# Kernel tuning notes

Hardware: AMD Instinct MI355X
Metric: run time of the kernel (lower is better)

The kernel has to match this reference:

```python
import jax, jax.numpy as jnp
import numpy as np

COMMITMENT_COST = 0.25


def setup_inputs() -> dict:
    key = jax.random.key(0)
    k1, k2 = jax.random.split(key)
    B, C, H, W, D = 8, 64, 32, 32, 32
    NUM_EMB = 512
    x = jax.random.normal(k1, (B, C, H, W, D), dtype=jnp.float32)
    # torch init: uniform(-1/num_embeddings, 1/num_embeddings)
    codebook = jax.random.uniform(k2, (NUM_EMB, C), dtype=jnp.float32,
                                  minval=-1.0 / NUM_EMB, maxval=1.0 / NUM_EMB)
    return {"x": x, "codebook": codebook}


def reference(x, codebook):
    B, C, H, W, D = x.shape
    # [B,C,H,W,D] -> [N, C] with N = B*H*W*D
    flat = jnp.transpose(x, (0, 2, 3, 4, 1)).reshape(-1, C)
    # squared L2 distances to every codebook entry: [N, num_embeddings]
    dist = (jnp.sum(flat * flat, axis=1, keepdims=True)
            - 2.0 * flat @ codebook.T
            + jnp.sum(codebook * codebook, axis=1))
    idx = jnp.argmin(dist, axis=1)                     # [N]
    # one-hot @ codebook  ==  gather (same math, efficient form)
    quant_flat = codebook[idx]                          # [N, C]
    quant = jnp.transpose(quant_flat.reshape(B, H, W, D, C), (0, 4, 1, 2, 3))
    e_loss = jnp.mean((jax.lax.stop_gradient(quant) - x) ** 2)
    q_loss = jnp.mean((quant - jax.lax.stop_gradient(x)) ** 2)
    loss = q_loss + COMMITMENT_COST * e_loss
    # straight-through estimator
    quant_st = x + jax.lax.stop_gradient(quant - x)
    return quant_st, loss
```

## Files before the change

### kernel.cpp

```cpp
#include <hip/hip_runtime.h>
#include <cstdint>
#include <cstddef>

#define SPATIAL   32768
#define CHANNELS  64
#define NUM_EMB   512
#define NPOS      262144
#define OUT_ELEMS 16777216
#define BLOCK     256
#define LOSS_SCALE (1.25f / 16777216.0f)

typedef __attribute__((ext_vector_type(8))) short bf16x8;
typedef __attribute__((ext_vector_type(4))) float f32x4;

union b8u { int i[4]; bf16x8 v; };
union fiu { float f; unsigned u; };

__device__ __forceinline__ short f2bf_rne(float f) {
    fiu v; v.f = f;
    unsigned r = v.u + 0x7fffu + ((v.u >> 16) & 1u);
    return (short)(r >> 16);
}

__global__ void vq_prep(const float* __restrict__ cb,
                        short* __restrict__ cbbf,
                        float* __restrict__ cbn,
                        float* __restrict__ loss_slot) {
    int e = blockIdx.x * blockDim.x + threadIdx.x;
    if (e == 0) *loss_slot = 0.0f;
    if (e < NUM_EMB) {
        float s = 0.0f;
#pragma unroll
        for (int c = 0; c < CHANNELS; ++c) {
            float v = cb[e * CHANNELS + c];
            cbbf[e * CHANNELS + c] = f2bf_rne(v);
            s = __builtin_fmaf(v, v, s);
        }
        cbn[e] = -0.5f * s;
    }
}

__global__ __launch_bounds__(BLOCK) void vq_main(
    const float* __restrict__ x,
    const float* __restrict__ cb,
    const short* __restrict__ cbbf,
    const float* __restrict__ cbn,
    float* __restrict__ out,
    float* __restrict__ loss_slot) {
#pragma clang fp contract(off)
    __shared__ int   cand[BLOCK];
    __shared__ float wsum[4];

    const int tid  = threadIdx.x;
    const int wave = tid >> 6, lane = tid & 63;
    const int q    = lane >> 4, col = lane & 15;

    const int blockPos = blockIdx.x * BLOCK;
    const int b     = blockPos >> 15;
    const int sbase = blockPos & 32767;
    const float* xb = x + (size_t)b * (CHANNELS * SPATIAL);
    const int wbase = sbase + wave * 64;

    b8u A[4][2];
#pragma unroll
    for (int t = 0; t < 4; ++t) {
        const unsigned* pu = (const unsigned*)xb + (wbase + t * 16 + col);
#pragma unroll
        for (int kh = 0; kh < 2; ++kh) {
#pragma unroll
            for (int jj = 0; jj < 4; ++jj) {
                unsigned u0 = pu[(size_t)(kh * 32 + q * 8 + 2 * jj + 0) * SPATIAL];
                unsigned u1 = pu[(size_t)(kh * 32 + q * 8 + 2 * jj + 1) * SPATIAL];
                A[t][kh].i[jj] = __builtin_amdgcn_perm(u1, u0, 0x07060302u);
            }
        }
    }

    float m[4][4];
#pragma unroll
    for (int t = 0; t < 4; ++t)
#pragma unroll
        for (int r = 0; r < 4; ++r) m[t][r] = -3.4e38f;

    const unsigned MASK = 0xFFFFFE00u;
    const int encBase = 511 - col;

    for (int nt = 0; nt < 32; ++nt) {
        const int e0 = nt * 16;
        const short* brow = cbbf + (size_t)(e0 + col) * CHANNELS + q * 8;
        bf16x8 B0 = *(const bf16x8*)(brow);
        bf16x8 B1 = *(const bf16x8*)(brow + 32);
        float cn = cbn[e0 + col];
        f32x4 ci = {cn, cn, cn, cn};
        const unsigned enc = (unsigned)(encBase - e0);
#pragma unroll
        for (int t = 0; t < 4; ++t) {
            f32x4 acc = __builtin_amdgcn_mfma_f32_16x16x32_bf16(A[t][0].v, B0, ci, 0, 0, 0);
            acc = __builtin_amdgcn_mfma_f32_16x16x32_bf16(A[t][1].v, B1, acc, 0, 0, 0);
#pragma unroll
            for (int r = 0; r < 4; ++r) {
                fiu p; p.f = acc[r];
                p.u = (p.u & MASK) | enc;
                m[t][r] = fmaxf(m[t][r], p.f);
            }
        }
    }

#pragma unroll
    for (int t = 0; t < 4; ++t) {
#pragma unroll
        for (int r = 0; r < 4; ++r) {
            float v = m[t][r];
#pragma unroll
            for (int d = 1; d < 16; d <<= 1)
                v = fmaxf(v, __shfl_xor(v, d, 64));
            if (col == 0) {
                fiu p; p.f = v;
                cand[wave * 64 + t * 16 + q * 4 + r] = 511 - (int)(p.u & 511u);
            }
        }
    }

    const int bidx = cand[tid];
    const float* qrow = cb + (size_t)bidx * CHANNELS;
    const float* px = xb + (sbase + tid);
    float* op = out + (size_t)b * (CHANNELS * SPATIAL) + (sbase + tid);
    float lsum = 0.0f;
#pragma unroll
    for (int c = 0; c < CHANNELS; ++c) {
        float xv = px[(size_t)c * SPATIAL];
        float t2 = qrow[c] - xv;
        op[(size_t)c * SPATIAL] = xv + t2;
        lsum = __builtin_fmaf(t2, t2, lsum);
    }

#pragma unroll
    for (int off = 32; off > 0; off >>= 1) lsum += __shfl_down(lsum, off, 64);
    if (lane == 0) wsum[wave] = lsum;
    __syncthreads();
    if (tid == 0) {
        float bs = (wsum[0] + wsum[1]) + (wsum[2] + wsum[3]);
        atomicAdd(loss_slot, bs * LOSS_SCALE);
    }
}

extern "C" void kernel_launch(void* const* d_in, const int* in_sizes, int n_in,
                              void* d_out, int out_size, void* d_ws, size_t ws_size,
                              hipStream_t stream) {
    const float* x  = (const float*)d_in[0];
    const float* cb = (const float*)d_in[1];
    float* out = (float*)d_out;
    short* cbbf = (short*)d_ws;
    float* cbn  = (float*)(cbbf + NUM_EMB * CHANNELS);
    float* loss_slot = out + OUT_ELEMS;

    vq_prep<<<2, 256, 0, stream>>>(cb, cbbf, cbn, loss_slot);
    vq_main<<<NPOS / BLOCK, BLOCK, 0, stream>>>(x, cb, cbbf, cbn, out, loss_slot);
}
```

Baseline: 156.3 us.

## Split codebook search across wave pairs and software-prefetch codebook tiles

Each block now handles 128 positions instead of 256. Two waves share each 64-position group, and each wave scans half of the codebook. The partial argmax results are merged through shared memory, and the epilogue splits the channels between the two halves of the block. The codebook B fragments and norms are also loaded one tile ahead to hide load latency. The aim is to shorten the serial MFMA/argmax chain per wave and double the block count for better occupancy and latency hiding. The cost is that each x tile is loaded twice, once per half-wave pair, and a block-wide sync is added.

```diff
diff --git a/kernel.cpp b/kernel.cpp
--- a/kernel.cpp
+++ b/kernel.cpp
@@ -8,6 +8,7 @@
 #define NPOS      262144
 #define OUT_ELEMS 16777216
 #define BLOCK     256
+#define POSB      128
 #define LOSS_SCALE (1.25f / 16777216.0f)
 
 typedef __attribute__((ext_vector_type(8))) short bf16x8;
@@ -48,23 +49,25 @@
     float* __restrict__ out,
     float* __restrict__ loss_slot) {
 #pragma clang fp contract(off)
-    __shared__ int   cand[BLOCK];
+    __shared__ float pm[2][POSB];
     __shared__ float wsum[4];
 
     const int tid  = threadIdx.x;
     const int wave = tid >> 6, lane = tid & 63;
     const int q    = lane >> 4, col = lane & 15;
+    const int posgrp = wave >> 1;
+    const int half   = wave & 1;
 
-    const int blockPos = blockIdx.x * BLOCK;
+    const int blockPos = blockIdx.x * POSB;
     const int b     = blockPos >> 15;
     const int sbase = blockPos & 32767;
     const float* xb = x + (size_t)b * (CHANNELS * SPATIAL);
-    const int wbase = sbase + wave * 64;
+    const int wposbase = sbase + posgrp * 64;
 
     b8u A[4][2];
 #pragma unroll
     for (int t = 0; t < 4; ++t) {
-        const unsigned* pu = (const unsigned*)xb + (wbase + t * 16 + col);
+        const unsigned* pu = (const unsigned*)xb + (wposbase + t * 16 + col);
 #pragma unroll
         for (int kh = 0; kh < 2; ++kh) {
 #pragma unroll
@@ -83,16 +86,22 @@
         for (int r = 0; r < 4; ++r) m[t][r] = -3.4e38f;
 
     const unsigned MASK = 0xFFFFFE00u;
-    const int encBase = 511 - col;
+    const int halfBase = half * 256;
+    const short* bbase = cbbf + (size_t)(halfBase + col) * CHANNELS + q * 8;
 
-    for (int nt = 0; nt < 32; ++nt) {
-        const int e0 = nt * 16;
-        const short* brow = cbbf + (size_t)(e0 + col) * CHANNELS + q * 8;
-        bf16x8 B0 = *(const bf16x8*)(brow);
-        bf16x8 B1 = *(const bf16x8*)(brow + 32);
-        float cn = cbn[e0 + col];
+    bf16x8 B0 = *(const bf16x8*)(bbase);
+    bf16x8 B1 = *(const bf16x8*)(bbase + 32);
+    float cn = cbn[halfBase + col];
+    for (int nt = 0; nt < 16; ++nt) {
+        bf16x8 nB0, nB1; float ncn;
+        if (nt < 15) {
+            const short* nb = bbase + (size_t)(nt + 1) * 16 * CHANNELS;
+            nB0 = *(const bf16x8*)(nb);
+            nB1 = *(const bf16x8*)(nb + 32);
+            ncn = cbn[halfBase + (nt + 1) * 16 + col];
+        }
         f32x4 ci = {cn, cn, cn, cn};
-        const unsigned enc = (unsigned)(encBase - e0);
+        const unsigned enc = (unsigned)(511 - (halfBase + nt * 16 + col));
 #pragma unroll
         for (int t = 0; t < 4; ++t) {
             f32x4 acc = __builtin_amdgcn_mfma_f32_16x16x32_bf16(A[t][0].v, B0, ci, 0, 0, 0);
@@ -104,6 +113,7 @@
                 m[t][r] = fmaxf(m[t][r], p.f);
             }
         }
+        if (nt < 15) { B0 = nB0; B1 = nB1; cn = ncn; }
     }
 
 #pragma unroll
@@ -114,20 +124,24 @@
 #pragma unroll
             for (int d = 1; d < 16; d <<= 1)
                 v = fmaxf(v, __shfl_xor(v, d, 64));
-            if (col == 0) {
-                fiu p; p.f = v;
-                cand[wave * 64 + t * 16 + q * 4 + r] = 511 - (int)(p.u & 511u);
-            }
+            if (col == 0)
+                pm[half][posgrp * 64 + t * 16 + q * 4 + r] = v;
         }
     }
+    __syncthreads();
 
-    const int bidx = cand[tid];
-    const float* qrow = cb + (size_t)bidx * CHANNELS;
-    const float* px = xb + (sbase + tid);
-    float* op = out + (size_t)b * (CHANNELS * SPATIAL) + (sbase + tid);
+    const int chalf = tid >> 7;
+    const int pos   = tid & 127;
+    fiu pk; pk.f = fmaxf(pm[0][pos], pm[1][pos]);
+    const int bidx = 511 - (int)(pk.u & 511u);
+
+    const float* qrow = cb + (size_t)bidx * CHANNELS + chalf * 32;
+    const float* px = xb + (sbase + pos) + (size_t)(chalf * 32) * SPATIAL;
+    float* op = out + (size_t)b * (CHANNELS * SPATIAL) + (sbase + pos)
+                    + (size_t)(chalf * 32) * SPATIAL;
     float lsum = 0.0f;
 #pragma unroll
-    for (int c = 0; c < CHANNELS; ++c) {
+    for (int c = 0; c < 32; ++c) {
         float xv = px[(size_t)c * SPATIAL];
         float t2 = qrow[c] - xv;
         op[(size_t)c * SPATIAL] = xv + t2;
@@ -155,5 +169,5 @@
     float* loss_slot = out + OUT_ELEMS;
 
     vq_prep<<<2, 256, 0, stream>>>(cb, cbbf, cbn, loss_slot);
-    vq_main<<<NPOS / BLOCK, BLOCK, 0, stream>>>(x, cb, cbbf, cbn, out, loss_slot);
+    vq_main<<<NPOS / POSB, BLOCK, 0, stream>>>(x, cb, cbbf, cbn, out, loss_slot);
 }
```

Result: slower. 195.0 us (+24.7%).
